# Performance work log

Measured on AMD Instinct MI355X. Metric: run time of the kernel, lower is better.

## Reference

```python
import jax, jax.numpy as jnp
import numpy as np

B, T_H, T_W, S_H, S_W = 64, 8, 8, 20, 20
DIM, HEADS = 768, 12
L = 2 * T_H * T_W + S_H * S_W  # 528


def setup_inputs() -> dict:
    key = jax.random.key(0)
    ks = jax.random.split(key, 6)
    sd = 0.02
    return {
        "x": jax.random.normal(ks[0], (B, L, DIM), jnp.float32),
        "Wq": jax.random.normal(ks[1], (DIM, DIM), jnp.float32) * sd,
        "Wk": jax.random.normal(ks[2], (DIM, DIM), jnp.float32) * sd,
        "Wv": jax.random.normal(ks[3], (DIM, DIM), jnp.float32) * sd,
        "Wp": jax.random.normal(ks[4], (DIM, DIM), jnp.float32) * sd,
        "bp": jnp.zeros((DIM,), jnp.float32),
        "t_h": T_H, "t_w": T_W, "s_h": S_H, "s_w": S_W,
    }


def _heads(y, h):
    b, t, d = y.shape
    return y.reshape(b, t, h, d // h).transpose(0, 2, 1, 3)  # b h t d


def _merge(y):
    b, h, t, d = y.shape
    return y.transpose(0, 2, 1, 3).reshape(b, t, h * d)


def _attn(q, k, v, scale):
    s = jnp.einsum("bhld,bhtd->bhlt", q, k) * scale
    p = jax.nn.softmax(s, axis=-1)
    return jnp.einsum("bhlt,bhtd->bhld", p, v)


def reference(x, Wq, Wk, Wv, Wp, bp, t_h, t_w, s_h, s_w):
    # forward_conv with default path is identity: q = k = v = x
    dim = Wq.shape[1]
    scale = dim ** (-0.5)  # NOTE: full dim_out, faithful to original
    q = _heads(x @ Wq, HEADS)
    k = _heads(x @ Wk, HEADS)
    v = _heads(x @ Wv, HEADS)
    Lt = t_h * t_w
    q_t, q_ot, q_s = q[:, :, :Lt], q[:, :, Lt:2 * Lt], q[:, :, 2 * Lt:]
    k12 = k[:, :, :2 * Lt]  # template+online keys
    v12 = v[:, :, :2 * Lt]
    x_t = _attn(q_t, k12, v12, scale)
    x_ot = _attn(q_ot, k12, v12, scale)
    x_s = _attn(q_s, k, v, scale)  # search attends to everything
    out = jnp.concatenate([_merge(x_t), _merge(x_ot), _merge(x_s)], axis=1)
    return out @ Wp + bp
```

## Files before the change

### kernel.cpp

```cpp
#include <hip/hip_runtime.h>
#include <stdint.h>

typedef __attribute__((ext_vector_type(8))) short bf16x8;
typedef __attribute__((ext_vector_type(4))) float f32x4;
typedef unsigned short ushort_t;
typedef unsigned int u32;
typedef const __attribute__((address_space(1))) u32* gp1_t;
typedef __attribute__((address_space(3))) u32* lp3_t;

#define MFMA(a,b,c) __builtin_amdgcn_mfma_f32_16x16x32_bf16((a),(b),(c),0,0,0)

static constexpr int BATCH = 64, LQ = 528, DIM = 768, NH = 12, DH = 64;
static constexpr int MTOK = BATCH * LQ;
static constexpr int VTP  = 544;
static constexpr float QSCALE = (float)(0.03608439182435161 * 1.4426950408889634);

__device__ __forceinline__ ushort_t f2bf(float f) {
  u32 u = __float_as_uint(f);
  u = (u + 0x7fffu + ((u >> 16) & 1u)) >> 16;
  return (ushort_t)u;
}
__device__ __forceinline__ u32 pack2(u32 xr, u32 yr) {
  return __builtin_amdgcn_perm(xr, yr, 0x07060302u);
}
__device__ __forceinline__ int swzK(int r) { return (r & 3) | (((r >> 3) & 1) << 2); }
__device__ __forceinline__ int swzV(int d) { return (d >> 2) & 3; }

__global__ __launch_bounds__(256) void k_convert_x(const float* __restrict__ x,
                                                   ushort_t* __restrict__ xb) {
  int i = blockIdx.x * 256 + threadIdx.x;
  float4 v = ((const float4*)x)[i];
  ushort4 o;
  o.x = f2bf(v.x); o.y = f2bf(v.y); o.z = f2bf(v.z); o.w = f2bf(v.w);
  ((ushort4*)xb)[i] = o;
}

__global__ __launch_bounds__(256) void k_convert_w(
    const float* __restrict__ w0, const float* __restrict__ w1,
    const float* __restrict__ w2, const float* __restrict__ w3,
    ushort_t* __restrict__ o0, ushort_t* __restrict__ o1,
    ushort_t* __restrict__ o2, ushort_t* __restrict__ o3) {
  __shared__ ushort_t t[64][65];
  int mid = blockIdx.z;
  const float* src = (mid == 0) ? w0 : (mid == 1) ? w1 : (mid == 2) ? w2 : w3;
  ushort_t* dst = (mid == 0) ? o0 : (mid == 1) ? o1 : (mid == 2) ? o2 : o3;
  int k0 = blockIdx.x * 64, n0 = blockIdx.y * 64;
  int c = threadIdx.x & 63, rr = threadIdx.x >> 6;
#pragma unroll
  for (int p = 0; p < 16; p++) {
    int r = p * 4 + rr;
    t[c][r] = f2bf(src[(size_t)(k0 + r) * DIM + n0 + c]);
  }
  __syncthreads();
#pragma unroll
  for (int p = 0; p < 16; p++) {
    int r = p * 4 + rr;
    dst[(size_t)(n0 + r) * DIM + k0 + c] = t[r][c];
  }
}

__global__ __launch_bounds__(512, 2) void k_gemm_qkv(
    const ushort_t* __restrict__ A, const ushort_t* __restrict__ wq,
    const ushort_t* __restrict__ wk, const ushort_t* __restrict__ wv,
    ushort_t* __restrict__ Qb, ushort_t* __restrict__ Kb, ushort_t* __restrict__ Vtb) {
  const int nwg = 1188, qq = nwg >> 3, rmn = nwg & 7;
  const int orig = blockIdx.x, xcd = orig & 7, within = orig >> 3;
  const int wgid = (xcd < rmn ? xcd * (qq + 1) : rmn * (qq + 1) + (xcd - rmn) * qq) + within;
  const int mT = wgid / 9, nT = wgid % 9;
  const int w = nT / 3, nc0 = (nT % 3) * 256;
  const ushort_t* Bt = (w == 0) ? wq : (w == 1) ? wk : wv;

  __shared__ ushort_t at[2][256 * 64];
  __shared__ ushort_t bt[2][256 * 64];
  const int tid = threadIdx.x;
  const int wid = tid >> 6, lane = tid & 63;
  const int lane15 = lane & 15, quad = lane >> 4;
  const int wm = wid >> 2, wn = wid & 3;
  const int lrow = lane >> 3, lchunk = lane & 7;

  f32x4 acc[8][4];
#pragma unroll
  for (int i = 0; i < 8; i++)
#pragma unroll
    for (int j = 0; j < 4; j++) acc[i][j] = (f32x4)0.0f;

  auto stage = [&](int p, int kt) {
    const int kb = kt * 64;
#pragma unroll
    for (int i = 0; i < 4; i++) {
      int r0 = i * 64 + wid * 8;
      int lr = r0 + lrow;
      size_t off = (size_t)(mT * 256 + lr) * 768 + kb + ((lchunk ^ (lr & 7)) << 3);
      __builtin_amdgcn_global_load_lds((gp1_t)(A + off), (lp3_t)(&at[p][r0 * 64]), 16, 0, 0);
    }
#pragma unroll
    for (int i = 0; i < 4; i++) {
      int r0 = i * 64 + wid * 8;
      int lr = r0 + lrow;
      size_t off = (size_t)(nc0 + lr) * 768 + kb + ((lchunk ^ (lr & 7)) << 3);
      __builtin_amdgcn_global_load_lds((gp1_t)(Bt + off), (lp3_t)(&bt[p][r0 * 64]), 16, 0, 0);
    }
  };

  stage(0, 0);
  asm volatile("s_waitcnt vmcnt(0)" ::: "memory");
  __builtin_amdgcn_s_barrier();
  __builtin_amdgcn_sched_barrier(0);

  for (int kt = 0; kt < 12; kt++) {
    const int p = kt & 1;
    if (kt + 1 < 12) stage(p ^ 1, kt + 1);

    bf16x8 bfr[4][2];
#pragma unroll
    for (int ni = 0; ni < 4; ni++)
#pragma unroll
      for (int h = 0; h < 2; h++) {
        int row = wn * 64 + ni * 16 + lane15;
        bfr[ni][h] = *(const bf16x8*)&bt[p][row * 64 + (((h * 4 + quad) ^ (row & 7)) << 3)];
      }

#pragma unroll
    for (int ph = 0; ph < 4; ph++) {
      bf16x8 af[2][2];
#pragma unroll
      for (int m2 = 0; m2 < 2; m2++)
#pragma unroll
        for (int h = 0; h < 2; h++) {
          int row = wm * 128 + (ph * 2 + m2) * 16 + lane15;
          af[m2][h] = *(const bf16x8*)&at[p][row * 64 + (((h * 4 + quad) ^ (row & 7)) << 3)];
        }
      __builtin_amdgcn_s_setprio(1);
#pragma unroll
      for (int m2 = 0; m2 < 2; m2++)
#pragma unroll
        for (int ni = 0; ni < 4; ni++) {
          acc[ph * 2 + m2][ni] = MFMA(af[m2][0], bfr[ni][0], acc[ph * 2 + m2][ni]);
          acc[ph * 2 + m2][ni] = MFMA(af[m2][1], bfr[ni][1], acc[ph * 2 + m2][ni]);
        }
      __builtin_amdgcn_s_setprio(0);
    }

    __builtin_amdgcn_sched_barrier(0);
    asm volatile("s_waitcnt vmcnt(0)" ::: "memory");
    __builtin_amdgcn_s_barrier();
    __builtin_amdgcn_sched_barrier(0);
  }

  const float scalev = (w == 0) ? QSCALE : 1.0f;
  ushort_t* Cqk = (w == 0) ? Qb : Kb;
#pragma unroll
  for (int mi = 0; mi < 8; mi++) {
#pragma unroll
    for (int rr = 0; rr < 4; rr++) {
      int m = mT * 256 + wm * 128 + mi * 16 + quad * 4 + rr;
      int b = m / 528, lt = m - b * 528;
#pragma unroll
      for (int ni = 0; ni < 4; ni++) {
        int n = nc0 + wn * 64 + ni * 16 + lane15;
        float v = acc[mi][ni][rr];
        if (w < 2) {
          Cqk[(((size_t)(b * 12 + (n >> 6)) * 528 + lt) << 6) + (n & 63)] = f2bf(v * scalev);
        } else {
          Vtb[((size_t)(b * 12 + (n >> 6)) * 64 + (n & 63)) * VTP + lt] = f2bf(v);
        }
      }
    }
  }
}

__global__ __launch_bounds__(256, 2) void k_gemm_out(const ushort_t* __restrict__ A,
                                                     const ushort_t* __restrict__ Bt,
                                                     float* __restrict__ C,
                                                     const float* __restrict__ bias) {
  const int id = blockIdx.x, xcd = id & 7, s = id >> 3;
  const int mT = xcd * 33 + s / 6, nT = s % 6;

  __shared__ ushort_t at[128 * 64];
  __shared__ ushort_t bt[128 * 64];
  const int tid = threadIdx.x;
  const int wv_ = tid >> 6, lane = tid & 63;
  const int lane15 = lane & 15, quad = lane >> 4;
  const int mw = (wv_ & 1) * 64, nw = (wv_ >> 1) * 64;

  f32x4 acc[4][4];
#pragma unroll
  for (int i = 0; i < 4; i++)
#pragma unroll
    for (int j = 0; j < 4; j++) acc[i][j] = (f32x4)0.0f;

  const int lrow = lane >> 3;
  const int lchunk = lane & 7;

  for (int kb = 0; kb < 768; kb += 64) {
#pragma unroll
    for (int i = 0; i < 4; i++) {
      int r0 = wv_ * 32 + i * 8;
      int lr = r0 + lrow;
      int grow = mT * 128 + lr;
      int gk = kb + ((lchunk ^ (lr & 7)) << 3);
      int b = grow / 528, ltk = grow - b * 528;
      size_t off = (((size_t)(b * 12 + (gk >> 6)) * 528 + ltk) << 6) + (gk & 63);
      __builtin_amdgcn_global_load_lds((gp1_t)(A + off), (lp3_t)(&at[r0 * 64]), 16, 0, 0);
    }
#pragma unroll
    for (int i = 0; i < 4; i++) {
      int r0 = wv_ * 32 + i * 8;
      int lr = r0 + lrow;
      size_t off = (size_t)(nT * 128 + lr) * 768 + kb + ((lchunk ^ (lr & 7)) << 3);
      __builtin_amdgcn_global_load_lds((gp1_t)(Bt + off), (lp3_t)(&bt[r0 * 64]), 16, 0, 0);
    }
    __syncthreads();
#pragma unroll
    for (int h = 0; h < 2; h++) {
      bf16x8 af[4], bf[4];
#pragma unroll
      for (int mi = 0; mi < 4; mi++) {
        int row = mw + mi * 16 + lane15;
        af[mi] = *(const bf16x8*)&at[row * 64 + (((h * 4 + quad) ^ (row & 7)) << 3)];
      }
#pragma unroll
      for (int ni = 0; ni < 4; ni++) {
        int row = nw + ni * 16 + lane15;
        bf[ni] = *(const bf16x8*)&bt[row * 64 + (((h * 4 + quad) ^ (row & 7)) << 3)];
      }
#pragma unroll
      for (int mi = 0; mi < 4; mi++)
#pragma unroll
        for (int ni = 0; ni < 4; ni++)
          acc[mi][ni] = MFMA(af[mi], bf[ni], acc[mi][ni]);
    }
    __syncthreads();
  }

#pragma unroll
  for (int mi = 0; mi < 4; mi++) {
#pragma unroll
    for (int r = 0; r < 4; r++) {
      int m = mT * 128 + mw + mi * 16 + quad * 4 + r;
#pragma unroll
      for (int ni = 0; ni < 4; ni++) {
        int n = nT * 128 + nw + ni * 16 + lane15;
        C[(size_t)m * 768 + n] = acc[mi][ni][r] + bias[n];
      }
    }
  }
}

__global__ __launch_bounds__(256, 3) void k_attn(ushort_t* __restrict__ Q,
                                                 const ushort_t* __restrict__ K,
                                                 const ushort_t* __restrict__ Vt) {
  __shared__ ushort_t Ksh[2][32 * 64];
  __shared__ ushort_t Vsh[2][64 * 32];
  const int tid = threadIdx.x;
  const int wv = tid >> 6, lane = tid & 63;
  const int lane15 = lane & 15, quad = lane >> 4;
  const int b = blockIdx.x, xcd = b & 7, slot = b >> 3;
  const int g = slot / 17, r = slot - g * 17;
  const int bh0 = (xcd * 24 + g) * 4;

  bf16x8 ones;
#pragma unroll
  for (int i = 0; i < 8; i++) ones[i] = (short)0x3F80;

  const int krp = ((lane15 >> 2) << 3) + (lane15 & 3);

  if (r < 16) {
    const int sub = r & 3;
    const int bh = bh0 + (r >> 2);
    const bool light = (sub == 3);
    const int rows0 = light ? (wv * 32) : (128 + sub * 128 + wv * 32);
    const int nch = light ? 4 : 17;

    ushort_t* Qb = Q + (size_t)bh * LQ * DH;
    const ushort_t* Kbh = K + (size_t)bh * LQ * DH;
    const ushort_t* Vbh = Vt + (size_t)bh * DH * VTP;

    bf16x8 aq[2][2];
#pragma unroll
    for (int mt = 0; mt < 2; mt++)
#pragma unroll
      for (int h = 0; h < 2; h++)
        aq[mt][h] = *(const bf16x8*)&Qb[(size_t)(rows0 + mt * 16 + lane15) * DH + h * 32 + quad * 8];

    f32x4 o[2][4], sm[2];
#pragma unroll
    for (int mt = 0; mt < 2; mt++) {
      sm[mt] = (f32x4)0.0f;
#pragma unroll
      for (int dt = 0; dt < 4; dt++) o[mt][dt] = (f32x4)0.0f;
    }

    auto stageKV = [&](int buf, int kc) {
      {
        int rr = tid >> 3, u = tid & 7;
        const ushort_t* src = Kbh + (size_t)(kc + rr) * DH + ((u ^ swzK(rr)) << 3);
        __builtin_amdgcn_global_load_lds((gp1_t)src, (lp3_t)&Ksh[buf][(wv * 8) * 64], 16, 0, 0);
      }
      {
        int d = tid >> 2, cc = tid & 3;
        const ushort_t* src = Vbh + (size_t)d * VTP + kc + ((cc ^ swzV(d)) << 3);
        __builtin_amdgcn_global_load_lds((gp1_t)src, (lp3_t)&Vsh[buf][(wv * 16) * 32], 16, 0, 0);
      }
    };

    stageKV(0, 0);
    for (int c = 0; c < nch; c++) {
      __syncthreads();
      if (c + 1 < nch) stageKV((c + 1) & 1, (c + 1) * 32);
      const int buf = c & 1;
      bf16x8 kf[2][2], vf[4];
#pragma unroll
      for (int ss = 0; ss < 2; ss++) {
        int kr = krp + ss * 4;
#pragma unroll
        for (int h = 0; h < 2; h++)
          kf[ss][h] = *(const bf16x8*)&Ksh[buf][kr * 64 + (((h * 4 + quad) ^ swzK(kr)) << 3)];
      }
#pragma unroll
      for (int dt = 0; dt < 4; dt++) {
        int d = dt * 16 + lane15;
        vf[dt] = *(const bf16x8*)&Vsh[buf][d * 32 + ((quad ^ swzV(d)) << 3)];
      }
      const bool maskl = (c == 16) && (quad >= 2);
#pragma unroll
      for (int mt = 0; mt < 2; mt++) {
        f32x4 c0 = (f32x4)0.0f, c1 = (f32x4)0.0f;
        c0 = MFMA(kf[0][0], aq[mt][0], c0);
        c0 = MFMA(kf[0][1], aq[mt][1], c0);
        c1 = MFMA(kf[1][0], aq[mt][0], c1);
        c1 = MFMA(kf[1][1], aq[mt][1], c1);
        u32 pw[8];
#pragma unroll
        for (int rr = 0; rr < 4; rr++) {
          float a0 = maskl ? -30.0f : c0[rr];
          float a1 = maskl ? -30.0f : c1[rr];
          pw[rr]     = __float_as_uint(exp2f(a0)) + 0x8000u;
          pw[4 + rr] = __float_as_uint(exp2f(a1)) + 0x8000u;
        }
        union { bf16x8 v; u32 w[4]; } pb;
        pb.w[0] = pack2(pw[1], pw[0]);
        pb.w[1] = pack2(pw[3], pw[2]);
        pb.w[2] = pack2(pw[5], pw[4]);
        pb.w[3] = pack2(pw[7], pw[6]);
        sm[mt] = MFMA(ones, pb.v, sm[mt]);
#pragma unroll
        for (int dt = 0; dt < 4; dt++)
          o[mt][dt] = MFMA(vf[dt], pb.v, o[mt][dt]);
      }
    }

#pragma unroll
    for (int mt = 0; mt < 2; mt++) {
      float inv = 1.0f / sm[mt][0];
      ushort_t* orow = &Qb[(size_t)(rows0 + mt * 16 + lane15) * DH];
#pragma unroll
      for (int dt = 0; dt < 4; dt++) {
        u32 r0 = __float_as_uint(o[mt][dt][0] * inv) + 0x8000u;
        u32 r1 = __float_as_uint(o[mt][dt][1] * inv) + 0x8000u;
        u32 r2 = __float_as_uint(o[mt][dt][2] * inv) + 0x8000u;
        u32 r3 = __float_as_uint(o[mt][dt][3] * inv) + 0x8000u;
        uint2 st;
        st.x = pack2(r1, r0);
        st.y = pack2(r3, r2);
        *(uint2*)&orow[dt * 16 + quad * 4] = st;
      }
    }
  } else {
    const int bh = bh0 + wv;
    ushort_t* Qb = Q + (size_t)bh * LQ * DH;
    const ushort_t* Kbh = K + (size_t)bh * LQ * DH;
    const ushort_t* Vbh = Vt + (size_t)bh * DH * VTP;

    bf16x8 aq[2];
#pragma unroll
    for (int h = 0; h < 2; h++)
      aq[h] = *(const bf16x8*)&Qb[(size_t)(512 + lane15) * DH + h * 32 + quad * 8];

    f32x4 o[4], sm = (f32x4)0.0f;
#pragma unroll
    for (int dt = 0; dt < 4; dt++) o[dt] = (f32x4)0.0f;

    const ushort_t* kbase = Kbh + (size_t)krp * DH + quad * 8;
    const ushort_t* vbase = Vbh + (size_t)lane15 * VTP + quad * 8;

    for (int kc = 0; kc < 528; kc += 32) {
      bf16x8 kf[2][2], vf[4];
#pragma unroll
      for (int ss = 0; ss < 2; ss++) {
        const ushort_t* p = kbase + (size_t)(kc + ss * 4) * DH;
        kf[ss][0] = *(const bf16x8*)&p[0];
        kf[ss][1] = *(const bf16x8*)&p[32];
      }
#pragma unroll
      for (int dt = 0; dt < 4; dt++)
        vf[dt] = *(const bf16x8*)&vbase[(size_t)dt * 16 * VTP + kc];

      f32x4 c0 = (f32x4)0.0f, c1 = (f32x4)0.0f;
      c0 = MFMA(kf[0][0], aq[0], c0);
      c0 = MFMA(kf[0][1], aq[1], c0);
      c1 = MFMA(kf[1][0], aq[0], c1);
      c1 = MFMA(kf[1][1], aq[1], c1);
      const bool maskl = (kc == 512) && (quad >= 2);
      u32 pw[8];
#pragma unroll
      for (int rr = 0; rr < 4; rr++) {
        float a0 = maskl ? -30.0f : c0[rr];
        float a1 = maskl ? -30.0f : c1[rr];
        pw[rr]     = __float_as_uint(exp2f(a0)) + 0x8000u;
        pw[4 + rr] = __float_as_uint(exp2f(a1)) + 0x8000u;
      }
      union { bf16x8 v; u32 w[4]; } pb;
      pb.w[0] = pack2(pw[1], pw[0]);
      pb.w[1] = pack2(pw[3], pw[2]);
      pb.w[2] = pack2(pw[5], pw[4]);
      pb.w[3] = pack2(pw[7], pw[6]);
      sm = MFMA(ones, pb.v, sm);
#pragma unroll
      for (int dt = 0; dt < 4; dt++)
        o[dt] = MFMA(vf[dt], pb.v, o[dt]);
    }

    float inv = 1.0f / sm[0];
    ushort_t* orow = &Qb[(size_t)(512 + lane15) * DH];
#pragma unroll
    for (int dt = 0; dt < 4; dt++) {
      u32 r0 = __float_as_uint(o[dt][0] * inv) + 0x8000u;
      u32 r1 = __float_as_uint(o[dt][1] * inv) + 0x8000u;
      u32 r2 = __float_as_uint(o[dt][2] * inv) + 0x8000u;
      u32 r3 = __float_as_uint(o[dt][3] * inv) + 0x8000u;
      uint2 st;
      st.x = pack2(r1, r0);
      st.y = pack2(r3, r2);
      *(uint2*)&orow[dt * 16 + quad * 4] = st;
    }
  }
}

extern "C" void kernel_launch(void* const* d_in, const int* in_sizes, int n_in,
                              void* d_out, int out_size, void* d_ws, size_t ws_size,
                              hipStream_t stream) {
  const float* x = (const float*)d_in[0];
  const float* Wq = (const float*)d_in[1];
  const float* Wk = (const float*)d_in[2];
  const float* Wv = (const float*)d_in[3];
  const float* Wp = (const float*)d_in[4];
  const float* bp = (const float*)d_in[5];
  float* out = (float*)d_out;

  char* ws = (char*)d_ws;
  size_t off = 0;
  auto alloc = [&](size_t bytes) {
    void* p = ws + off;
    off += (bytes + 255) & ~(size_t)255;
    return p;
  };
  ushort_t* xb = (ushort_t*)alloc((size_t)MTOK * DIM * 2);
  ushort_t* wtq = (ushort_t*)alloc((size_t)DIM * DIM * 2);
  ushort_t* wtk = (ushort_t*)alloc((size_t)DIM * DIM * 2);
  ushort_t* wtv = (ushort_t*)alloc((size_t)DIM * DIM * 2);
  ushort_t* wtp = (ushort_t*)alloc((size_t)DIM * DIM * 2);
  ushort_t* Qb = (ushort_t*)alloc((size_t)MTOK * DIM * 2);
  ushort_t* Kb = (ushort_t*)alloc((size_t)MTOK * DIM * 2);
  ushort_t* Vtb = (ushort_t*)alloc((size_t)BATCH * NH * DH * VTP * 2);
  (void)ws_size; (void)in_sizes; (void)n_in; (void)out_size;

  k_convert_x<<<25344, 256, 0, stream>>>(x, xb);
  k_convert_w<<<dim3(12, 12, 4), 256, 0, stream>>>(Wq, Wk, Wv, Wp, wtq, wtk, wtv, wtp);
  k_gemm_qkv<<<1188, 512, 0, stream>>>(xb, wtq, wtk, wtv, Qb, Kb, Vtb);
  k_attn<<<3264, 256, 0, stream>>>(Qb, Kb, Vtb);
  k_gemm_out<<<1584, 256, 0, stream>>>(Qb, wtp, out, bp);
}
```

Before: 572.6 us.

## Pipeline QKV GEMM at half-K granularity and double-buffer output projection GEMM

The QKV projection GEMM now splits each 64-wide K step into four 32-wide half-tiles (A and B for each half). The loads for the next stage are issued between MFMA phases, with vmcnt-based waits and barriers in place of one full wait per K step, and a new swizzle suits the 32-element rows. The output projection GEMM gets double-buffered LDS so the next K tile loads while the current one computes. The aim is to hide global-to-LDS load latency behind MFMA work, at the cost of more complex synchronisation and more LDS in the out-GEMM.

```diff
diff --git a/kernel.cpp b/kernel.cpp
--- a/kernel.cpp
+++ b/kernel.cpp
@@ -63,20 +63,17 @@
     const ushort_t* __restrict__ A, const ushort_t* __restrict__ wq,
     const ushort_t* __restrict__ wk, const ushort_t* __restrict__ wv,
     ushort_t* __restrict__ Qb, ushort_t* __restrict__ Kb, ushort_t* __restrict__ Vtb) {
-  const int nwg = 1188, qq = nwg >> 3, rmn = nwg & 7;
   const int orig = blockIdx.x, xcd = orig & 7, within = orig >> 3;
-  const int wgid = (xcd < rmn ? xcd * (qq + 1) : rmn * (qq + 1) + (xcd - rmn) * qq) + within;
-  const int mT = wgid / 9, nT = wgid % 9;
-  const int w = nT / 3, nc0 = (nT % 3) * 256;
+  const int wgid = (xcd < 4 ? xcd * 149 : 4 * 149 + (xcd - 4) * 148) + within;
+  const int mT = wgid / 9, nT9 = wgid % 9;
+  const int w = nT9 / 3, nc0 = (nT9 % 3) * 256;
   const ushort_t* Bt = (w == 0) ? wq : (w == 1) ? wk : wv;
 
-  __shared__ ushort_t at[2][256 * 64];
-  __shared__ ushort_t bt[2][256 * 64];
+  __shared__ ushort_t smem[2][4][8192];
   const int tid = threadIdx.x;
   const int wid = tid >> 6, lane = tid & 63;
   const int lane15 = lane & 15, quad = lane >> 4;
   const int wm = wid >> 2, wn = wid & 3;
-  const int lrow = lane >> 3, lchunk = lane & 7;
 
   f32x4 acc[8][4];
 #pragma unroll
@@ -84,68 +81,140 @@
 #pragma unroll
     for (int j = 0; j < 4; j++) acc[i][j] = (f32x4)0.0f;
 
-  auto stage = [&](int p, int kt) {
-    const int kb = kt * 64;
-#pragma unroll
-    for (int i = 0; i < 4; i++) {
-      int r0 = i * 64 + wid * 8;
-      int lr = r0 + lrow;
-      size_t off = (size_t)(mT * 256 + lr) * 768 + kb + ((lchunk ^ (lr & 7)) << 3);
-      __builtin_amdgcn_global_load_lds((gp1_t)(A + off), (lp3_t)(&at[p][r0 * 64]), 16, 0, 0);
-    }
-#pragma unroll
-    for (int i = 0; i < 4; i++) {
-      int r0 = i * 64 + wid * 8;
-      int lr = r0 + lrow;
-      size_t off = (size_t)(nc0 + lr) * 768 + kb + ((lchunk ^ (lr & 7)) << 3);
-      __builtin_amdgcn_global_load_lds((gp1_t)(Bt + off), (lp3_t)(&bt[p][r0 * 64]), 16, 0, 0);
+  auto stageH = [&](int sl, int u, int kt) {
+    const int kb = kt * 64 + ((u >> 1) << 5);
+    const ushort_t* src = (u & 1) ? Bt : A;
+    const int rb = (u & 1) ? nc0 : mT * 256;
+#pragma unroll
+    for (int j = 0; j < 2; j++) {
+      int row = j * 128 + (tid >> 2);
+      int c = tid & 3;
+      size_t off = (size_t)(rb + row) * 768 + kb + ((c ^ ((row >> 1) & 3)) << 3);
+      __builtin_amdgcn_global_load_lds((gp1_t)(src + off),
+          (lp3_t)&smem[sl][u][(j * 128 + wid * 16) * 32], 16, 0, 0);
     }
   };
-
-  stage(0, 0);
-  asm volatile("s_waitcnt vmcnt(0)" ::: "memory");
-  __builtin_amdgcn_s_barrier();
-  __builtin_amdgcn_sched_barrier(0);
-
-  for (int kt = 0; kt < 12; kt++) {
-    const int p = kt & 1;
-    if (kt + 1 < 12) stage(p ^ 1, kt + 1);
-
-    bf16x8 bfr[4][2];
-#pragma unroll
-    for (int ni = 0; ni < 4; ni++)
-#pragma unroll
-      for (int h = 0; h < 2; h++) {
-        int row = wn * 64 + ni * 16 + lane15;
-        bfr[ni][h] = *(const bf16x8*)&bt[p][row * 64 + (((h * 4 + quad) ^ (row & 7)) << 3)];
-      }
-
-#pragma unroll
-    for (int ph = 0; ph < 4; ph++) {
-      bf16x8 af[2][2];
-#pragma unroll
-      for (int m2 = 0; m2 < 2; m2++)
-#pragma unroll
-        for (int h = 0; h < 2; h++) {
-          int row = wm * 128 + (ph * 2 + m2) * 16 + lane15;
-          af[m2][h] = *(const bf16x8*)&at[p][row * 64 + (((h * 4 + quad) ^ (row & 7)) << 3)];
-        }
-      __builtin_amdgcn_s_setprio(1);
-#pragma unroll
-      for (int m2 = 0; m2 < 2; m2++)
-#pragma unroll
-        for (int ni = 0; ni < 4; ni++) {
-          acc[ph * 2 + m2][ni] = MFMA(af[m2][0], bfr[ni][0], acc[ph * 2 + m2][ni]);
-          acc[ph * 2 + m2][ni] = MFMA(af[m2][1], bfr[ni][1], acc[ph * 2 + m2][ni]);
-        }
-      __builtin_amdgcn_s_setprio(0);
-    }
-
-    __builtin_amdgcn_sched_barrier(0);
-    asm volatile("s_waitcnt vmcnt(0)" ::: "memory");
-    __builtin_amdgcn_s_barrier();
-    __builtin_amdgcn_sched_barrier(0);
-  }
+  auto rdA = [&](int sl, int h, int mi) {
+    int row = wm * 128 + mi * 16 + lane15;
+    return *(const bf16x8*)&smem[sl][h * 2][row * 32 + ((quad ^ ((row >> 1) & 3)) << 3)];
+  };
+  auto rdB = [&](int sl, int h, int ni) {
+    int row = wn * 64 + ni * 16 + lane15;
+    return *(const bf16x8*)&smem[sl][h * 2 + 1][row * 32 + ((quad ^ ((row >> 1) & 3)) << 3)];
+  };
+
+#define VMCNT4 asm volatile("s_waitcnt vmcnt(4)" ::: "memory")
+#define VMCNT0 asm volatile("s_waitcnt vmcnt(0)" ::: "memory")
+#define SBAR   __builtin_amdgcn_s_barrier()
+#define SCHED0 __builtin_amdgcn_sched_barrier(0)
+#define PRIO1  __builtin_amdgcn_s_setprio(1)
+#define PRIO0  __builtin_amdgcn_s_setprio(0)
+
+  stageH(0, 0, 0); stageH(0, 1, 0); stageH(0, 2, 0); stageH(0, 3, 0);
+
+  for (int t = 0; t < 11; t++) {
+    const int sl = t & 1, so = sl ^ 1;
+    bf16x8 af[4], bf[4];
+    VMCNT4; SBAR; SCHED0;
+#pragma unroll
+    for (int i = 0; i < 4; i++) af[i] = rdA(sl, 0, i);
+#pragma unroll
+    for (int i = 0; i < 4; i++) bf[i] = rdB(sl, 0, i);
+    stageH(so, 0, t + 1);
+    SCHED0; PRIO1;
+#pragma unroll
+    for (int mi = 0; mi < 4; mi++)
+#pragma unroll
+      for (int ni = 0; ni < 4; ni++)
+        acc[mi][ni] = MFMA(af[mi], bf[ni], acc[mi][ni]);
+    PRIO0; SCHED0;
+    SBAR; SCHED0;
+#pragma unroll
+    for (int i = 0; i < 4; i++) af[i] = rdA(sl, 0, 4 + i);
+    stageH(so, 1, t + 1);
+    SCHED0; PRIO1;
+#pragma unroll
+    for (int mi = 0; mi < 4; mi++)
+#pragma unroll
+      for (int ni = 0; ni < 4; ni++)
+        acc[4 + mi][ni] = MFMA(af[mi], bf[ni], acc[4 + mi][ni]);
+    PRIO0; SCHED0;
+    VMCNT4; SBAR; SCHED0;
+#pragma unroll
+    for (int i = 0; i < 4; i++) af[i] = rdA(sl, 1, i);
+#pragma unroll
+    for (int i = 0; i < 4; i++) bf[i] = rdB(sl, 1, i);
+    stageH(so, 2, t + 1);
+    SCHED0; PRIO1;
+#pragma unroll
+    for (int mi = 0; mi < 4; mi++)
+#pragma unroll
+      for (int ni = 0; ni < 4; ni++)
+        acc[mi][ni] = MFMA(af[mi], bf[ni], acc[mi][ni]);
+    PRIO0; SCHED0;
+    SBAR; SCHED0;
+#pragma unroll
+    for (int i = 0; i < 4; i++) af[i] = rdA(sl, 1, 4 + i);
+    stageH(so, 3, t + 1);
+    SCHED0; PRIO1;
+#pragma unroll
+    for (int mi = 0; mi < 4; mi++)
+#pragma unroll
+      for (int ni = 0; ni < 4; ni++)
+        acc[4 + mi][ni] = MFMA(af[mi], bf[ni], acc[4 + mi][ni]);
+    PRIO0; SCHED0;
+  }
+  {
+    bf16x8 af[4], bf[4];
+    VMCNT4; SBAR; SCHED0;
+#pragma unroll
+    for (int i = 0; i < 4; i++) af[i] = rdA(1, 0, i);
+#pragma unroll
+    for (int i = 0; i < 4; i++) bf[i] = rdB(1, 0, i);
+    PRIO1;
+#pragma unroll
+    for (int mi = 0; mi < 4; mi++)
+#pragma unroll
+      for (int ni = 0; ni < 4; ni++)
+        acc[mi][ni] = MFMA(af[mi], bf[ni], acc[mi][ni]);
+    PRIO0; SCHED0;
+#pragma unroll
+    for (int i = 0; i < 4; i++) af[i] = rdA(1, 0, 4 + i);
+    PRIO1;
+#pragma unroll
+    for (int mi = 0; mi < 4; mi++)
+#pragma unroll
+      for (int ni = 0; ni < 4; ni++)
+        acc[4 + mi][ni] = MFMA(af[mi], bf[ni], acc[4 + mi][ni]);
+    PRIO0; SCHED0;
+    VMCNT0; SBAR; SCHED0;
+#pragma unroll
+    for (int i = 0; i < 4; i++) af[i] = rdA(1, 1, i);
+#pragma unroll
+    for (int i = 0; i < 4; i++) bf[i] = rdB(1, 1, i);
+    PRIO1;
+#pragma unroll
+    for (int mi = 0; mi < 4; mi++)
+#pragma unroll
+      for (int ni = 0; ni < 4; ni++)
+        acc[mi][ni] = MFMA(af[mi], bf[ni], acc[mi][ni]);
+    PRIO0; SCHED0;
+#pragma unroll
+    for (int i = 0; i < 4; i++) af[i] = rdA(1, 1, 4 + i);
+    PRIO1;
+#pragma unroll
+    for (int mi = 0; mi < 4; mi++)
+#pragma unroll
+      for (int ni = 0; ni < 4; ni++)
+        acc[4 + mi][ni] = MFMA(af[mi], bf[ni], acc[4 + mi][ni]);
+    PRIO0; SCHED0;
+  }
+#undef VMCNT4
+#undef VMCNT0
+#undef SBAR
+#undef SCHED0
+#undef PRIO1
+#undef PRIO0
 
   const float scalev = (w == 0) ? QSCALE : 1.0f;
   ushort_t* Cqk = (w == 0) ? Qb : Kb;
@@ -176,8 +245,8 @@
   const int id = blockIdx.x, xcd = id & 7, s = id >> 3;
   const int mT = xcd * 33 + s / 6, nT = s % 6;
 
-  __shared__ ushort_t at[128 * 64];
-  __shared__ ushort_t bt[128 * 64];
+  __shared__ ushort_t at[2][128 * 64];
+  __shared__ ushort_t bt[2][128 * 64];
   const int tid = threadIdx.x;
   const int wv_ = tid >> 6, lane = tid & 63;
   const int lane15 = lane & 15, quad = lane >> 4;
@@ -192,7 +261,7 @@
   const int lrow = lane >> 3;
   const int lchunk = lane & 7;
 
-  for (int kb = 0; kb < 768; kb += 64) {
+  auto stage = [&](int p, int kb) {
 #pragma unroll
     for (int i = 0; i < 4; i++) {
       int r0 = wv_ * 32 + i * 8;
@@ -201,28 +270,36 @@
       int gk = kb + ((lchunk ^ (lr & 7)) << 3);
       int b = grow / 528, ltk = grow - b * 528;
       size_t off = (((size_t)(b * 12 + (gk >> 6)) * 528 + ltk) << 6) + (gk & 63);
-      __builtin_amdgcn_global_load_lds((gp1_t)(A + off), (lp3_t)(&at[r0 * 64]), 16, 0, 0);
+      __builtin_amdgcn_global_load_lds((gp1_t)(A + off), (lp3_t)(&at[p][r0 * 64]), 16, 0, 0);
     }
 #pragma unroll
     for (int i = 0; i < 4; i++) {
       int r0 = wv_ * 32 + i * 8;
       int lr = r0 + lrow;
       size_t off = (size_t)(nT * 128 + lr) * 768 + kb + ((lchunk ^ (lr & 7)) << 3);
-      __builtin_amdgcn_global_load_lds((gp1_t)(Bt + off), (lp3_t)(&bt[r0 * 64]), 16, 0, 0);
-    }
-    __syncthreads();
+      __builtin_amdgcn_global_load_lds((gp1_t)(Bt + off), (lp3_t)(&bt[p][r0 * 64]), 16, 0, 0);
+    }
+  };
+
+  stage(0, 0);
+  __syncthreads();
+
+  for (int kt = 0; kt < 12; kt++) {
+    const int p = kt & 1;
+    if (kt < 11) stage(p ^ 1, (kt + 1) * 64);
+    __builtin_amdgcn_sched_barrier(0);
 #pragma unroll
     for (int h = 0; h < 2; h++) {
       bf16x8 af[4], bf[4];
 #pragma unroll
       for (int mi = 0; mi < 4; mi++) {
         int row = mw + mi * 16 + lane15;
-        af[mi] = *(const bf16x8*)&at[row * 64 + (((h * 4 + quad) ^ (row & 7)) << 3)];
+        af[mi] = *(const bf16x8*)&at[p][row * 64 + (((h * 4 + quad) ^ (row & 7)) << 3)];
       }
 #pragma unroll
       for (int ni = 0; ni < 4; ni++) {
         int row = nw + ni * 16 + lane15;
-        bf[ni] = *(const bf16x8*)&bt[row * 64 + (((h * 4 + quad) ^ (row & 7)) << 3)];
+        bf[ni] = *(const bf16x8*)&bt[p][row * 64 + (((h * 4 + quad) ^ (row & 7)) << 3)];
       }
 #pragma unroll
       for (int mi = 0; mi < 4; mi++)
```

Result: faster. 537.5 us (-6.1%).
